# Kernel optimization log

Measured on AMD Instinct MI355X. Metric: run time of the kernel, lower is better.

Reference implementation:

```python
import jax, jax.numpy as jnp
from jax import lax
import numpy as np

IN_C = 256
PREV_IN_C = 256
OUT_C = 128
ATTN = IN_C // 8  # attn_size == attn_out == 32


def setup_inputs() -> dict:
    key = jax.random.key(0)
    ks = jax.random.split(key, 12)
    B, W, H = 4, 64, 64
    s = 0.02
    return {
        "source_enc_f": jax.random.normal(ks[0], (B, IN_C, W, H), jnp.float32),
        "target_enc_f": jax.random.normal(ks[1], (B, IN_C, W, H), jnp.float32),
        "prev_inp": jax.random.normal(ks[2], (B, PREV_IN_C, W // 2, H // 2), jnp.float32),
        "key_w": s * jax.random.normal(ks[3], (ATTN, IN_C), jnp.float32),
        "key_b": jnp.zeros((ATTN,), jnp.float32),
        "query_w": s * jax.random.normal(ks[4], (ATTN, IN_C), jnp.float32),
        "query_b": jnp.zeros((ATTN,), jnp.float32),
        "lin_w": s * jax.random.normal(ks[5], (ATTN, 2 * ATTN), jnp.float32),  # k_q_linear: cat([key, query])
        "lin_b": jnp.zeros((ATTN,), jnp.float32),
        "attn_w": s * jax.random.normal(ks[6], (IN_C, ATTN + IN_C), jnp.float32),
        "attn_b": jnp.zeros((IN_C,), jnp.float32),
        "gamma": jnp.array(0.1, jnp.float32),  # torch inits 0.0; nonzero so attn path is exercised
        "conv_w": s * jax.random.normal(ks[7], (OUT_C, IN_C + PREV_IN_C, 3, 3), jnp.float32),
        "conv_b": jnp.zeros((OUT_C,), jnp.float32),
    }


def _forward(source_enc_f, target_enc_f, prev_inp, key_w, key_b, query_w, query_b,
             lin_w, lin_b, attn_w, attn_b, gamma, conv_w, conv_b):
    B, C, W, H = source_enc_f.shape
    WH = W * H
    A = ATTN
    # 1x1 convs for query/key
    q = jnp.einsum('oc,bchw->bohw', query_w, source_enc_f) + query_b[:, None, None]
    k = jnp.einsum('oc,bchw->bohw', key_w, target_enc_f) + key_b[:, None, None]
    # Original: for every (key pos a, query pos c) pair, Linear(cat(key[a], query[c])),
    # then sum over c. Linear is separable: out[a] = WH*(Wk@key[a] + b) + Wq @ sum_c query[c].
    Wk, Wq = lin_w[:, :A], lin_w[:, A:]
    key_term = jnp.einsum('oa,bahw->bohw', Wk, k)          # [B, attn_out, W, H]
    q_sum = jnp.einsum('oa,ba->bo', Wq, q.sum(axis=(2, 3)))  # [B, attn_out]
    attn_map = WH * (key_term + lin_b[:, None, None]) + q_sum[:, :, None, None]
    # attn_conv (1x1) over cat([target, attn_map])
    x = jnp.concatenate([target_enc_f, attn_map], axis=1)
    out = jnp.einsum('oc,bchw->bohw', attn_w, x) + attn_b[:, None, None]
    x = target_enc_f + gamma * out
    prev_up = jnp.repeat(jnp.repeat(prev_inp, 2, axis=2), 2, axis=3)
    x = jnp.concatenate([x, prev_up], axis=1)
    y = lax.conv_general_dilated(x, conv_w, (1, 1), 'SAME',
                                 dimension_numbers=('NCHW', 'OIHW', 'NCHW'))
    y = y + conv_b[:, None, None]
    mean = y.mean(axis=(2, 3), keepdims=True)
    var = y.var(axis=(2, 3), keepdims=True)  # biased, as torch InstanceNorm2d
    y = (y - mean) * lax.rsqrt(var + 1e-5)
    return jax.nn.relu(y)


def reference(source_enc_f, target_enc_f, prev_inp, key_w, key_b, query_w, query_b,
              lin_w, lin_b, attn_w, attn_b, gamma, conv_w, conv_b):
    return _forward(source_enc_f, target_enc_f, prev_inp, key_w, key_b, query_w, query_b,
                    lin_w, lin_b, attn_w, attn_b, gamma, conv_w, conv_b)
```

## Files before the change

### kernel.cpp

```cpp
#include <hip/hip_runtime.h>

typedef unsigned short u16;
typedef __attribute__((ext_vector_type(8))) __bf16 bf16x8;
typedef __attribute__((ext_vector_type(8))) unsigned short u16x8;
typedef __attribute__((ext_vector_type(4))) float f32x4;

__device__ __forceinline__ u16 f2bf(float f) {
  unsigned u = __builtin_bit_cast(unsigned, f);
  unsigned r = u + 0x7fffu + ((u >> 16) & 1u);
  return (u16)(r >> 16);
}

__device__ __forceinline__ float wave_sum(float v) {
#pragma unroll
  for (int o = 32; o; o >>= 1) v += __shfl_xor(v, o, 64);
  return v;
}

__device__ __forceinline__ void gl2lds16(const u16* g, u16* l) {
  __builtin_amdgcn_global_load_lds(
      (const __attribute__((address_space(1))) unsigned int*)(const void*)g,
      (__attribute__((address_space(3))) unsigned int*)(void*)l, 16, 0, 0);
}

__global__ void k0(const float* __restrict__ src, const float* __restrict__ kw,
                   const float* __restrict__ lw, const float* __restrict__ aw,
                   const float* __restrict__ gamma,
                   float* __restrict__ ssum, float* __restrict__ Mt) {
  __shared__ float red[64];
  int tid = threadIdx.x;
  if (blockIdx.x >= 1024) {
    int o = blockIdx.x - 1024;
    if (tid < 32) {
      float s = 0.f;
      for (int o2 = 0; o2 < 32; ++o2) s += aw[o * 288 + 256 + o2] * lw[o2 * 64 + tid];
      red[tid] = s;
    }
    __syncthreads();
    float s = 0.f;
    for (int a = 0; a < 32; ++a) s += red[a] * kw[a * 256 + tid];
    Mt[o * 256 + tid] = gamma[0] * (aw[o * 288 + tid] + 4096.f * s) + (o == tid ? 1.f : 0.f);
    return;
  }
  int plane = blockIdx.x;
  const float* p = src + (size_t)plane * 4096;
  float s = 0.f;
#pragma unroll
  for (int i = 0; i < 4; ++i) {
    f32x4 v = *(const f32x4*)(p + (i * 256 + tid) * 4);
    s += v[0] + v[1] + v[2] + v[3];
  }
  s = wave_sum(s);
  if ((tid & 63) == 0) red[tid >> 6] = s;
  __syncthreads();
  if (tid == 0) ssum[plane] = red[0] + red[1] + red[2] + red[3];
}

__global__ void k1(const float* __restrict__ tgt, const float* __restrict__ prev,
                   const float* __restrict__ cw, const float* __restrict__ Mt,
                   const float* __restrict__ ssum,
                   const float* __restrict__ qw, const float* __restrict__ qb,
                   const float* __restrict__ kb, const float* __restrict__ lw,
                   const float* __restrict__ lb, const float* __restrict__ aw,
                   const float* __restrict__ ab, const float* __restrict__ gamma,
                   u16* __restrict__ xin, u16* __restrict__ w3,
                   float* __restrict__ cd2) {
  __shared__ __align__(16) unsigned char smem[49152];
  int tid = threadIdx.x;
  if (blockIdx.x < 36) {
    float* S = (float*)smem;
    float* part = S;
    float* qs = S + 512;
    float* amap = S + 544;
    float* dvec = S + 576;
    int b = blockIdx.x / 9;
    int pbase = (blockIdx.x % 9) * 128;
    {
      int o = tid >> 4, seg = tid & 15;
      float s = 0.f;
#pragma unroll
      for (int i = 0; i < 16; ++i) {
        int c = seg * 16 + i;
        s += qw[o * 256 + c] * ssum[b * 256 + c];
      }
      part[tid] = s;
    }
    __syncthreads();
    if (tid < 32) {
      float s = 4096.f * qb[tid];
#pragma unroll
      for (int k = 0; k < 16; ++k) s += part[tid * 16 + k];
      qs[tid] = s;
    }
    __syncthreads();
    if (tid < 32) {
      int o2 = tid;
      float s = 0.f, kt = 0.f;
#pragma unroll
      for (int o = 0; o < 32; ++o) {
        s += lw[o2 * 64 + 32 + o] * qs[o];
        kt += lw[o2 * 64 + o] * kb[o];
      }
      amap[o2] = 4096.f * (kt + lb[o2]) + s;
    }
    __syncthreads();
    if (tid < 256) {
      float s = ab[tid];
#pragma unroll
      for (int o2 = 0; o2 < 32; ++o2) s += aw[tid * 288 + 256 + o2] * amap[o2];
      dvec[tid] = gamma[0] * s;
    }
    __syncthreads();
    {
      int grp = tid >> 2, q = tid & 3;
      int p = pbase + grp;
      int oc = p / 9, tap = p - oc * 9;
      const float* cwp = cw + (size_t)(oc * 512) * 9 + tap;
      float s0 = 0.f, s1 = 0.f, s2 = 0.f, s3 = 0.f;
#pragma unroll
      for (int i = 0; i < 16; ++i) {
        int c = q * 64 + i * 4;
        s0 += cwp[(size_t)c * 9] * dvec[c];
        s1 += cwp[(size_t)(c + 1) * 9] * dvec[c + 1];
        s2 += cwp[(size_t)(c + 2) * 9] * dvec[c + 2];
        s3 += cwp[(size_t)(c + 3) * 9] * dvec[c + 3];
      }
      float s = (s0 + s1) + (s2 + s3);
      s += __shfl_xor(s, 1, 64);
      s += __shfl_xor(s, 2, 64);
      if (q == 0) cd2[(size_t)(b * 128 + oc) * 9 + tap] = s;
    }
    return;
  }
  if (blockIdx.x < 180) {
    float* cwl = (float*)smem;
    float* mtile = (float*)smem + 4096;
    int blk = blockIdx.x - 36;
    int tap = blk >> 4, ocg = blk & 15;
    for (int e = tid; e < 4096; e += 512) {
      int oc = e >> 9, c = e & 511;
      cwl[e] = cw[(size_t)((ocg * 8 + oc) * 512 + c) * 9 + tap];
    }
    int wv = tid >> 6, l = tid & 63;
    int c2 = l * 4;
    f32x4 acc = {0.f, 0.f, 0.f, 0.f};
    for (int cb = 0; cb < 8; ++cb) {
      __syncthreads();
#pragma unroll
      for (int i = 0; i < 4; ++i) {
        int e = i * 512 + tid;
        ((f32x4*)mtile)[e] = *(const f32x4*)(Mt + cb * 8192 + e * 4);
      }
      __syncthreads();
#pragma unroll
      for (int cc = 0; cc < 32; ++cc) {
        float wc = cwl[wv * 512 + cb * 32 + cc];
        f32x4 m = *(const f32x4*)(mtile + cc * 256 + c2);
#pragma unroll
        for (int j = 0; j < 4; ++j) acc[j] += wc * m[j];
      }
    }
    int ocf = ocg * 8 + wv;
#pragma unroll
    for (int j2 = 0; j2 < 4; ++j2) {
      int cf = c2 + j2;
      w3[(tap * 16 + (cf >> 5)) * 4096 + ((cf >> 3) & 3) * 1024 + ocf * 8 + (cf & 7)] = f2bf(acc[j2]);
      cf = 256 + c2 + j2;
      w3[(tap * 16 + (cf >> 5)) * 4096 + ((cf >> 3) & 3) * 1024 + ocf * 8 + (cf & 7)] =
          f2bf(cwl[wv * 512 + (c2 + j2 + 256)]);
    }
    return;
  }
  u16* lt = (u16*)smem;
  int bi = blockIdx.x - 180;
  int b = bi >> 6, h = bi & 63;
  u16* slab = xin + (size_t)(b * 64 + h) * 40960;
  if (tid < 256) {
    int cg = tid >> 4, colidx = tid & 15;
    int pxp = (colidx == 0) ? 0 : (64 + colidx);
    u16x8 zz;
#pragma unroll
    for (int q = 0; q < 8; ++q) zz[q] = 0;
    u16* d = slab + cg * 2560 + pxp * 32;
    *(u16x8*)(d) = zz; *(u16x8*)(d + 8) = zz;
    *(u16x8*)(d + 16) = zz; *(u16x8*)(d + 24) = zz;
  }
#pragma unroll
  for (int it = 0; it < 8; ++it) {
    int fi = it * 512 + tid;
    int c = fi >> 4, w4 = fi & 15;
    f32x4 v = *(const f32x4*)(tgt + ((size_t)(b * 256 + c) * 64 + h) * 64 + w4 * 4);
    int base = c * 66 + w4 * 4;
    lt[base] = f2bf(v[0]); lt[base + 1] = f2bf(v[1]);
    lt[base + 2] = f2bf(v[2]); lt[base + 3] = f2bf(v[3]);
  }
  __syncthreads();
  {
    int cg = tid >> 6, l = tid & 63;
    int s = l & 3;
#pragma unroll
    for (int it = 0; it < 4; ++it) {
      int pxp = 1 + it * 16 + (l >> 2);
      int g = s ^ ((pxp >> 1) & 3);
      int o = cg * 4 + g;
      int w = pxp - 1;
      u16x8 v;
#pragma unroll
      for (int k = 0; k < 8; ++k) v[k] = lt[(o * 8 + k) * 66 + w];
      *(u16x8*)(slab + cg * 2560 + pxp * 32 + s * 8) = v;
    }
  }
  __syncthreads();
#pragma unroll
  for (int it = 0; it < 4; ++it) {
    int pi = it * 512 + tid;
    int cc = pi >> 3, wq = pi & 7;
    f32x4 v = *(const f32x4*)(prev + ((size_t)(b * 256 + cc) * 32 + (h >> 1)) * 32 + wq * 4);
    int base = cc * 66 + wq * 8;
    u16 b0 = f2bf(v[0]), b1 = f2bf(v[1]), b2 = f2bf(v[2]), b3 = f2bf(v[3]);
    lt[base] = b0; lt[base + 1] = b0; lt[base + 2] = b1; lt[base + 3] = b1;
    lt[base + 4] = b2; lt[base + 5] = b2; lt[base + 6] = b3; lt[base + 7] = b3;
  }
  __syncthreads();
  {
    int cg8 = tid >> 6, l = tid & 63;
    int s = l & 3;
#pragma unroll
    for (int it = 0; it < 4; ++it) {
      int pxp = 1 + it * 16 + (l >> 2);
      int g = s ^ ((pxp >> 1) & 3);
      int o = cg8 * 4 + g;
      int w = pxp - 1;
      u16x8 v;
#pragma unroll
      for (int k = 0; k < 8; ++k) v[k] = lt[(o * 8 + k) * 66 + w];
      *(u16x8*)(slab + (8 + cg8) * 2560 + pxp * 32 + s * 8) = v;
    }
  }
}

__global__ __launch_bounds__(512) void k_conv(const u16* __restrict__ xin,
                                              const u16* __restrict__ w3,
                                              const float* __restrict__ cd2,
                                              float* __restrict__ out) {
  __shared__ u16 lds[52736];
  const int XIN0 = 36864, DUMMY = 52224;
  int bid = blockIdx.x;
  int lid = (bid & 7) * 32 + (bid >> 3);
  int b = lid >> 6, h = lid & 63;
  int tid = threadIdx.x, l = tid & 63, wv = tid >> 6;
  int wr = wv & 3, wpx = wv >> 2;
  int r = l & 15, kb4 = l >> 4;

  if (h == 0 || h == 63) {
    int row = (h == 0) ? 0 : 2;
    for (int i = tid; i < 640; i += 512) {
      int bu = i / 320, off = (i % 320) * 8;
      u16x8 zz;
#pragma unroll
      for (int q = 0; q < 8; ++q) zz[q] = 0;
      *(u16x8*)(lds + XIN0 + bu * 7680 + row * 2560 + off) = zz;
    }
  }

  auto ISSUE_W3 = [&](int c2, int dy2, int buf, bool dummy) {
    u16* dst0 = lds + buf * 12288;
#pragma unroll
    for (int i = 0; i < 3; ++i) {
      int k = wv + 8 * i;
      int dx = k >> 3, part = k & 7;
      const u16* src = dummy ? (w3 + l * 8)
          : (w3 + (size_t)(((dy2 * 3 + dx) * 16 + c2) << 12) + part * 512 + l * 8);
      u16* dst = dummy ? (lds + DUMMY) : (dst0 + dx * 4096 + part * 512);
      gl2lds16(src, dst);
    }
  };
  auto ISSUE_XIN = [&](int c1, int buf, bool dummyAll) {
    u16* dst0 = lds + XIN0 + buf * 7680;
#pragma unroll
    for (int i = 0; i < 2; ++i) {
      int k = wv + 8 * i;
      int row = k / 5, part = k - row * 5;
      int grow = h - 1 + row;
      bool dm = dummyAll || (k == 15) || ((unsigned)grow >= 64u);
      const u16* src = dm ? (xin + l * 8)
          : (xin + ((size_t)(b * 64 + grow) * 16 + c1) * 2560 + part * 512 + l * 8);
      u16* dst = dm ? (lds + DUMMY) : (dst0 + row * 2560 + part * 512);
      gl2lds16(src, dst);
    }
  };

  f32x4 acc[2][2];
#pragma unroll
  for (int mf = 0; mf < 2; ++mf)
#pragma unroll
    for (int nf = 0; nf < 2; ++nf) acc[mf][nf] = f32x4{0.f, 0.f, 0.f, 0.f};

  ISSUE_W3(0, 0, 0, false);
  ISSUE_XIN(0, 0, false);
  ISSUE_W3(0, 1, 1, false);

  for (int c = 0; c < 16; ++c) {
#pragma unroll
    for (int dy = 0; dy < 3; ++dy) {
      if (dy == 0) asm volatile("s_waitcnt vmcnt(3) lgkmcnt(0)" ::: "memory");
      else         asm volatile("s_waitcnt vmcnt(5) lgkmcnt(0)" ::: "memory");
      __builtin_amdgcn_s_barrier();
      __builtin_amdgcn_sched_barrier(0);
      {
        int c2 = c + ((dy + 2) / 3);
        ISSUE_W3(c2, (dy + 2) % 3, (dy + 2) % 3, c2 > 15);
      }
      if (dy == 0) ISSUE_XIN(c + 1, (c + 1) & 1, c + 1 > 15);
      const u16* wbuf = lds + dy * 12288;
      const u16* xrow = lds + XIN0 + (c & 1) * 7680 + dy * 2560;
      __builtin_amdgcn_s_setprio(1);
#pragma unroll
      for (int dx = 0; dx < 3; ++dx) {
        bf16x8 av[2];
#pragma unroll
        for (int mf = 0; mf < 2; ++mf)
          av[mf] = *(const bf16x8*)(wbuf + dx * 4096 + kb4 * 1024 + (wr * 32 + mf * 16 + r) * 8);
        bf16x8 bv[2];
#pragma unroll
        for (int nf = 0; nf < 2; ++nf) {
          int pxp = wpx * 32 + nf * 16 + r + dx;
          int slot = kb4 ^ ((pxp >> 1) & 3);
          bv[nf] = *(const bf16x8*)(xrow + pxp * 32 + slot * 8);
        }
#pragma unroll
        for (int mf = 0; mf < 2; ++mf)
#pragma unroll
          for (int nf = 0; nf < 2; ++nf)
            acc[mf][nf] = __builtin_amdgcn_mfma_f32_16x16x32_bf16(av[mf], bv[nf], acc[mf][nf], 0, 0, 0);
      }
      __builtin_amdgcn_s_setprio(0);
    }
  }

  bool dy0v = (h > 0), dy2v = (h < 63);
#pragma unroll
  for (int mf = 0; mf < 2; ++mf) {
#pragma unroll
    for (int j = 0; j < 4; ++j) {
      int oc = wr * 32 + mf * 16 + kb4 * 4 + j;
      const float* cd = cd2 + (size_t)(b * 128 + oc) * 9;
      float sAll = 0.f, sL = 0.f, sR = 0.f;
#pragma unroll
      for (int dy3 = 0; dy3 < 3; ++dy3) {
        bool v = (dy3 == 1) || (dy3 == 0 ? dy0v : dy2v);
        if (v) {
          sAll += cd[dy3 * 3] + cd[dy3 * 3 + 1] + cd[dy3 * 3 + 2];
          sL += cd[dy3 * 3];
          sR += cd[dy3 * 3 + 2];
        }
      }
#pragma unroll
      for (int nf = 0; nf < 2; ++nf) {
        int px = wpx * 32 + nf * 16 + r;
        float corr = sAll - (px == 0 ? sL : 0.f) - (px == 63 ? sR : 0.f);
        out[(size_t)(b * 128 + oc) * 4096 + h * 64 + px] = acc[mf][nf][j] + corr;
      }
    }
  }
}

__global__ void k_norm(float* __restrict__ out) {
  int plane = blockIdx.x;
  float* p = out + (size_t)plane * 4096;
  int t = threadIdx.x;
  f32x4 v[4];
  float s = 0.f, s2 = 0.f;
#pragma unroll
  for (int i = 0; i < 4; ++i) {
    v[i] = *(const f32x4*)(p + (i * 256 + t) * 4);
#pragma unroll
    for (int k = 0; k < 4; ++k) { s += v[i][k]; s2 += v[i][k] * v[i][k]; }
  }
  s = wave_sum(s); s2 = wave_sum(s2);
  __shared__ float rs[4], rs2[4];
  if ((t & 63) == 0) { rs[t >> 6] = s; rs2[t >> 6] = s2; }
  __syncthreads();
  float S = rs[0] + rs[1] + rs[2] + rs[3];
  float S2 = rs2[0] + rs2[1] + rs2[2] + rs2[3];
  float mean = S * (1.f / 4096.f);
  float var = S2 * (1.f / 4096.f) - mean * mean;
  float inv = rsqrtf(var + 1e-5f);
#pragma unroll
  for (int i = 0; i < 4; ++i) {
    f32x4 o;
#pragma unroll
    for (int k = 0; k < 4; ++k) {
      float y = (v[i][k] - mean) * inv;
      o[k] = y > 0.f ? y : 0.f;
    }
    *(f32x4*)(p + (i * 256 + t) * 4) = o;
  }
}

extern "C" void kernel_launch(void* const* d_in, const int* in_sizes, int n_in,
                              void* d_out, int out_size, void* d_ws, size_t ws_size,
                              hipStream_t stream) {
  const float* src    = (const float*)d_in[0];
  const float* tgt    = (const float*)d_in[1];
  const float* prev   = (const float*)d_in[2];
  const float* key_w  = (const float*)d_in[3];
  const float* key_b  = (const float*)d_in[4];
  const float* qry_w  = (const float*)d_in[5];
  const float* qry_b  = (const float*)d_in[6];
  const float* lin_w  = (const float*)d_in[7];
  const float* lin_b  = (const float*)d_in[8];
  const float* attn_w = (const float*)d_in[9];
  const float* attn_b = (const float*)d_in[10];
  const float* gamma  = (const float*)d_in[11];
  const float* conv_w = (const float*)d_in[12];

  char* ws = (char*)d_ws;
  size_t off = 0;
  u16*   xin  = (u16*)(ws + off);  off += 20971520;
  float* ssum = (float*)(ws + off); off += 4096;
  float* Mt   = (float*)(ws + off); off += 262144;
  float* cd2  = (float*)(ws + off); off += 18432;
  u16*   w3   = (u16*)(ws + off);  off += 1179648;
  float* out  = (float*)d_out;

  k0<<<1280, 256, 0, stream>>>(src, key_w, lin_w, attn_w, gamma, ssum, Mt);
  k1<<<436, 512, 0, stream>>>(tgt, prev, conv_w, Mt, ssum, qry_w, qry_b, key_b,
                              lin_w, lin_b, attn_w, attn_b, gamma, xin, w3, cd2);
  k_conv<<<256, 512, 0, stream>>>(xin, w3, cd2, out);
  k_norm<<<512, 256, 0, stream>>>(out);
}
```

Before: 60.82 us.

## Move input packing blocks from k1 into k0 to rebalance kernel stages

The bf16 packing of target and upsampled prev inputs into the padded xin slab moves from k1 into k0, where it runs alongside the spatial-sum and Mt blocks. k0 now uses 512 threads per block, with the plane-sum loop and reduction adjusted to match. k1 keeps only the dvec/cd2 and w3 weight-fold blocks, so its critical path is shorter. The aim is to overlap the bandwidth-heavy packing with the independent k0 work instead of with the Mt-dependent k1 work, at the cost of a larger LDS footprint for every k0 block.

```diff
diff --git a/kernel.cpp b/kernel.cpp
--- a/kernel.cpp
+++ b/kernel.cpp
@@ -26,45 +26,123 @@
 __global__ void k0(const float* __restrict__ src, const float* __restrict__ kw,
                    const float* __restrict__ lw, const float* __restrict__ aw,
                    const float* __restrict__ gamma,
-                   float* __restrict__ ssum, float* __restrict__ Mt) {
-  __shared__ float red[64];
+                   const float* __restrict__ tgt, const float* __restrict__ prev,
+                   float* __restrict__ ssum, float* __restrict__ Mt,
+                   u16* __restrict__ xin) {
+  __shared__ __align__(16) unsigned char smem[33792];
   int tid = threadIdx.x;
+  if (blockIdx.x >= 1280) {
+    u16* lt = (u16*)smem;
+    int bi = blockIdx.x - 1280;
+    int b = bi >> 6, h = bi & 63;
+    u16* slab = xin + (size_t)(b * 64 + h) * 40960;
+    if (tid < 256) {
+      int cg = tid >> 4, colidx = tid & 15;
+      int pxp = (colidx == 0) ? 0 : (64 + colidx);
+      u16x8 zz;
+#pragma unroll
+      for (int q = 0; q < 8; ++q) zz[q] = 0;
+      u16* d = slab + cg * 2560 + pxp * 32;
+      *(u16x8*)(d) = zz; *(u16x8*)(d + 8) = zz;
+      *(u16x8*)(d + 16) = zz; *(u16x8*)(d + 24) = zz;
+    }
+#pragma unroll
+    for (int it = 0; it < 8; ++it) {
+      int fi = it * 512 + tid;
+      int c = fi >> 4, w4 = fi & 15;
+      f32x4 v = *(const f32x4*)(tgt + ((size_t)(b * 256 + c) * 64 + h) * 64 + w4 * 4);
+      int base = c * 66 + w4 * 4;
+      lt[base] = f2bf(v[0]); lt[base + 1] = f2bf(v[1]);
+      lt[base + 2] = f2bf(v[2]); lt[base + 3] = f2bf(v[3]);
+    }
+    __syncthreads();
+    {
+      int cg = tid >> 6, l = tid & 63;
+      int s = l & 3;
+#pragma unroll
+      for (int it = 0; it < 4; ++it) {
+        int pxp = 1 + it * 16 + (l >> 2);
+        int g = s ^ ((pxp >> 1) & 3);
+        int o = cg * 4 + g;
+        int w = pxp - 1;
+        u16x8 v;
+#pragma unroll
+        for (int k = 0; k < 8; ++k) v[k] = lt[(o * 8 + k) * 66 + w];
+        *(u16x8*)(slab + cg * 2560 + pxp * 32 + s * 8) = v;
+      }
+    }
+    __syncthreads();
+#pragma unroll
+    for (int it = 0; it < 4; ++it) {
+      int pi = it * 512 + tid;
+      int cc = pi >> 3, wq = pi & 7;
+      f32x4 v = *(const f32x4*)(prev + ((size_t)(b * 256 + cc) * 32 + (h >> 1)) * 32 + wq * 4);
+      int base = cc * 66 + wq * 8;
+      u16 b0 = f2bf(v[0]), b1 = f2bf(v[1]), b2 = f2bf(v[2]), b3 = f2bf(v[3]);
+      lt[base] = b0; lt[base + 1] = b0; lt[base + 2] = b1; lt[base + 3] = b1;
+      lt[base + 4] = b2; lt[base + 5] = b2; lt[base + 6] = b3; lt[base + 7] = b3;
+    }
+    __syncthreads();
+    {
+      int cg8 = tid >> 6, l = tid & 63;
+      int s = l & 3;
+#pragma unroll
+      for (int it = 0; it < 4; ++it) {
+        int pxp = 1 + it * 16 + (l >> 2);
+        int g = s ^ ((pxp >> 1) & 3);
+        int o = cg8 * 4 + g;
+        int w = pxp - 1;
+        u16x8 v;
+#pragma unroll
+        for (int k = 0; k < 8; ++k) v[k] = lt[(o * 8 + k) * 66 + w];
+        *(u16x8*)(slab + (8 + cg8) * 2560 + pxp * 32 + s * 8) = v;
+      }
+    }
+    return;
+  }
   if (blockIdx.x >= 1024) {
+    float* E = (float*)smem;
     int o = blockIdx.x - 1024;
     if (tid < 32) {
       float s = 0.f;
       for (int o2 = 0; o2 < 32; ++o2) s += aw[o * 288 + 256 + o2] * lw[o2 * 64 + tid];
-      red[tid] = s;
-    }
-    __syncthreads();
-    float s = 0.f;
-    for (int a = 0; a < 32; ++a) s += red[a] * kw[a * 256 + tid];
-    Mt[o * 256 + tid] = gamma[0] * (aw[o * 288 + tid] + 4096.f * s) + (o == tid ? 1.f : 0.f);
+      E[tid] = s;
+    }
+    __syncthreads();
+    if (tid < 256) {
+      float s = 0.f;
+      for (int a = 0; a < 32; ++a) s += E[a] * kw[a * 256 + tid];
+      Mt[o * 256 + tid] = gamma[0] * (aw[o * 288 + tid] + 4096.f * s) + (o == tid ? 1.f : 0.f);
+    }
     return;
   }
+  float* red = (float*)smem;
   int plane = blockIdx.x;
   const float* p = src + (size_t)plane * 4096;
   float s = 0.f;
 #pragma unroll
-  for (int i = 0; i < 4; ++i) {
-    f32x4 v = *(const f32x4*)(p + (i * 256 + tid) * 4);
+  for (int i = 0; i < 2; ++i) {
+    f32x4 v = *(const f32x4*)(p + i * 2048 + tid * 4);
     s += v[0] + v[1] + v[2] + v[3];
   }
   s = wave_sum(s);
   if ((tid & 63) == 0) red[tid >> 6] = s;
   __syncthreads();
-  if (tid == 0) ssum[plane] = red[0] + red[1] + red[2] + red[3];
-}
-
-__global__ void k1(const float* __restrict__ tgt, const float* __restrict__ prev,
-                   const float* __restrict__ cw, const float* __restrict__ Mt,
+  if (tid == 0) {
+    float t = 0.f;
+#pragma unroll
+    for (int i = 0; i < 8; ++i) t += red[i];
+    ssum[plane] = t;
+  }
+}
+
+__global__ void k1(const float* __restrict__ cw, const float* __restrict__ Mt,
                    const float* __restrict__ ssum,
                    const float* __restrict__ qw, const float* __restrict__ qb,
                    const float* __restrict__ kb, const float* __restrict__ lw,
                    const float* __restrict__ lb, const float* __restrict__ aw,
                    const float* __restrict__ ab, const float* __restrict__ gamma,
-                   u16* __restrict__ xin, u16* __restrict__ w3,
-                   float* __restrict__ cd2) {
+                   u16* __restrict__ w3, float* __restrict__ cd2) {
   __shared__ __align__(16) unsigned char smem[49152];
   int tid = threadIdx.x;
   if (blockIdx.x < 36) {
@@ -132,110 +210,41 @@
     }
     return;
   }
-  if (blockIdx.x < 180) {
-    float* cwl = (float*)smem;
-    float* mtile = (float*)smem + 4096;
-    int blk = blockIdx.x - 36;
-    int tap = blk >> 4, ocg = blk & 15;
-    for (int e = tid; e < 4096; e += 512) {
-      int oc = e >> 9, c = e & 511;
-      cwl[e] = cw[(size_t)((ocg * 8 + oc) * 512 + c) * 9 + tap];
-    }
-    int wv = tid >> 6, l = tid & 63;
-    int c2 = l * 4;
-    f32x4 acc = {0.f, 0.f, 0.f, 0.f};
-    for (int cb = 0; cb < 8; ++cb) {
-      __syncthreads();
-#pragma unroll
-      for (int i = 0; i < 4; ++i) {
-        int e = i * 512 + tid;
-        ((f32x4*)mtile)[e] = *(const f32x4*)(Mt + cb * 8192 + e * 4);
-      }
-      __syncthreads();
-#pragma unroll
-      for (int cc = 0; cc < 32; ++cc) {
-        float wc = cwl[wv * 512 + cb * 32 + cc];
-        f32x4 m = *(const f32x4*)(mtile + cc * 256 + c2);
-#pragma unroll
-        for (int j = 0; j < 4; ++j) acc[j] += wc * m[j];
-      }
-    }
-    int ocf = ocg * 8 + wv;
-#pragma unroll
-    for (int j2 = 0; j2 < 4; ++j2) {
-      int cf = c2 + j2;
-      w3[(tap * 16 + (cf >> 5)) * 4096 + ((cf >> 3) & 3) * 1024 + ocf * 8 + (cf & 7)] = f2bf(acc[j2]);
-      cf = 256 + c2 + j2;
-      w3[(tap * 16 + (cf >> 5)) * 4096 + ((cf >> 3) & 3) * 1024 + ocf * 8 + (cf & 7)] =
-          f2bf(cwl[wv * 512 + (c2 + j2 + 256)]);
-    }
-    return;
-  }
-  u16* lt = (u16*)smem;
-  int bi = blockIdx.x - 180;
-  int b = bi >> 6, h = bi & 63;
-  u16* slab = xin + (size_t)(b * 64 + h) * 40960;
-  if (tid < 256) {
-    int cg = tid >> 4, colidx = tid & 15;
-    int pxp = (colidx == 0) ? 0 : (64 + colidx);
-    u16x8 zz;
-#pragma unroll
-    for (int q = 0; q < 8; ++q) zz[q] = 0;
-    u16* d = slab + cg * 2560 + pxp * 32;
-    *(u16x8*)(d) = zz; *(u16x8*)(d + 8) = zz;
-    *(u16x8*)(d + 16) = zz; *(u16x8*)(d + 24) = zz;
-  }
-#pragma unroll
-  for (int it = 0; it < 8; ++it) {
-    int fi = it * 512 + tid;
-    int c = fi >> 4, w4 = fi & 15;
-    f32x4 v = *(const f32x4*)(tgt + ((size_t)(b * 256 + c) * 64 + h) * 64 + w4 * 4);
-    int base = c * 66 + w4 * 4;
-    lt[base] = f2bf(v[0]); lt[base + 1] = f2bf(v[1]);
-    lt[base + 2] = f2bf(v[2]); lt[base + 3] = f2bf(v[3]);
-  }
-  __syncthreads();
-  {
-    int cg = tid >> 6, l = tid & 63;
-    int s = l & 3;
-#pragma unroll
-    for (int it = 0; it < 4; ++it) {
-      int pxp = 1 + it * 16 + (l >> 2);
-      int g = s ^ ((pxp >> 1) & 3);
-      int o = cg * 4 + g;
-      int w = pxp - 1;
-      u16x8 v;
-#pragma unroll
-      for (int k = 0; k < 8; ++k) v[k] = lt[(o * 8 + k) * 66 + w];
-      *(u16x8*)(slab + cg * 2560 + pxp * 32 + s * 8) = v;
-    }
-  }
-  __syncthreads();
-#pragma unroll
-  for (int it = 0; it < 4; ++it) {
-    int pi = it * 512 + tid;
-    int cc = pi >> 3, wq = pi & 7;
-    f32x4 v = *(const f32x4*)(prev + ((size_t)(b * 256 + cc) * 32 + (h >> 1)) * 32 + wq * 4);
-    int base = cc * 66 + wq * 8;
-    u16 b0 = f2bf(v[0]), b1 = f2bf(v[1]), b2 = f2bf(v[2]), b3 = f2bf(v[3]);
-    lt[base] = b0; lt[base + 1] = b0; lt[base + 2] = b1; lt[base + 3] = b1;
-    lt[base + 4] = b2; lt[base + 5] = b2; lt[base + 6] = b3; lt[base + 7] = b3;
-  }
-  __syncthreads();
-  {
-    int cg8 = tid >> 6, l = tid & 63;
-    int s = l & 3;
-#pragma unroll
-    for (int it = 0; it < 4; ++it) {
-      int pxp = 1 + it * 16 + (l >> 2);
-      int g = s ^ ((pxp >> 1) & 3);
-      int o = cg8 * 4 + g;
-      int w = pxp - 1;
-      u16x8 v;
-#pragma unroll
-      for (int k = 0; k < 8; ++k) v[k] = lt[(o * 8 + k) * 66 + w];
-      *(u16x8*)(slab + (8 + cg8) * 2560 + pxp * 32 + s * 8) = v;
-    }
+  float* cwl = (float*)smem;
+  float* mtile = (float*)smem + 4096;
+  int blk = blockIdx.x - 36;
+  int tap = blk >> 4, ocg = blk & 15;
+  for (int e = tid; e < 4096; e += 512) {
+    int oc = e >> 9, c = e & 511;
+    cwl[e] = cw[(size_t)((ocg * 8 + oc) * 512 + c) * 9 + tap];
+  }
+  int wv = tid >> 6, l = tid & 63;
+  int c2 = l * 4;
+  f32x4 acc = {0.f, 0.f, 0.f, 0.f};
+  for (int cb = 0; cb < 8; ++cb) {
+    __syncthreads();
+#pragma unroll
+    for (int i = 0; i < 4; ++i) {
+      int e = i * 512 + tid;
+      ((f32x4*)mtile)[e] = *(const f32x4*)(Mt + cb * 8192 + e * 4);
+    }
+    __syncthreads();
+#pragma unroll
+    for (int cc = 0; cc < 32; ++cc) {
+      float wc = cwl[wv * 512 + cb * 32 + cc];
+      f32x4 m = *(const f32x4*)(mtile + cc * 256 + c2);
+#pragma unroll
+      for (int j = 0; j < 4; ++j) acc[j] += wc * m[j];
+    }
+  }
+  int ocf = ocg * 8 + wv;
+#pragma unroll
+  for (int j2 = 0; j2 < 4; ++j2) {
+    int cf = c2 + j2;
+    w3[(tap * 16 + (cf >> 5)) * 4096 + ((cf >> 3) & 3) * 1024 + ocf * 8 + (cf & 7)] = f2bf(acc[j2]);
+    cf = 256 + c2 + j2;
+    w3[(tap * 16 + (cf >> 5)) * 4096 + ((cf >> 3) & 3) * 1024 + ocf * 8 + (cf & 7)] =
+        f2bf(cwl[wv * 512 + (c2 + j2 + 256)]);
   }
 }
 
@@ -424,9 +433,10 @@
   u16*   w3   = (u16*)(ws + off);  off += 1179648;
   float* out  = (float*)d_out;
 
-  k0<<<1280, 256, 0, stream>>>(src, key_w, lin_w, attn_w, gamma, ssum, Mt);
-  k1<<<436, 512, 0, stream>>>(tgt, prev, conv_w, Mt, ssum, qry_w, qry_b, key_b,
-                              lin_w, lin_b, attn_w, attn_b, gamma, xin, w3, cd2);
+  k0<<<1536, 512, 0, stream>>>(src, key_w, lin_w, attn_w, gamma, tgt, prev,
+                               ssum, Mt, xin);
+  k1<<<180, 512, 0, stream>>>(conv_w, Mt, ssum, qry_w, qry_b, key_b, lin_w, lin_b,
+                              attn_w, attn_b, gamma, w3, cd2);
   k_conv<<<256, 512, 0, stream>>>(xin, w3, cd2, out);
   k_norm<<<512, 256, 0, stream>>>(out);
 }
```

New measurement: 67.55 us. +11.1%, slower.
